# Optimization experiments

Measured on AMD Instinct MI355X. Metric: run time of the kernel, lower is better.

## Reference

```python
import jax, jax.numpy as jnp
import numpy as np

T = 64        # time steps (batch)
N_SIDE = 256  # grid side, N = N_SIDE**2 flattened grid points
HID = 32      # hidden width of the shared per-point MLP
IN_CH = 5     # 5-point periodic stencil (l, l2, center, r, r2)


def _stencil_gather(x, n):
    """Replicates MLPConv._preprocess / make_px / get_value exactly.

    x: [T, n*n] flattened periodic grid. Returns [T, n*n, 5].
    get_value wraps indices via the piecewise rule (v-n if v>=n) and relies on
    numpy negative flat indexing for v=-1, which is the final `% (n*n)` here.
    Output position i_loop*n + j_loop reads grid flat index (j_loop+ik) + n*(i_loop+jk).
    """
    ii = jnp.arange(n)[:, None]  # i_loop (outer loop in make_px)
    jj = jnp.arange(n)[None, :]  # j_loop (inner loop)

    def idx(ik, jk):
        a = jj + ik
        a = jnp.where(a >= n, a - n, a)
        b = ii + jk
        b = jnp.where(b >= n, b - n, b)
        return ((a + n * b) % (n * n)).reshape(-1)  # [n*n]

    # channel order from _preprocess: cat([l, l2, px, r, r2], -1)
    offsets = [(-1, 0), (0, -1), (0, 0), (1, 0), (0, 1)]
    cols = jnp.stack([idx(ik, jk) for ik, jk in offsets], axis=-1)  # [n*n, 5]
    return x[:, cols]  # [T, n*n, 5]


def setup_inputs() -> dict:
    key = jax.random.key(0)
    ks = jax.random.split(key, 7)
    n2 = N_SIDE * N_SIDE
    x = jax.random.normal(ks[0], (T, n2), dtype=jnp.float32)
    # torch Linear weights are [out, in]; we store transposed [in, out] for x @ W.
    # Original init: xavier_normal * 10, bias zeros; scaled normals are equivalent for a baseline.
    def w(k, fan_in, fan_out):
        std = 10.0 * np.sqrt(2.0 / (fan_in + fan_out))
        return std * jax.random.normal(k, (fan_in, fan_out), dtype=jnp.float32)
    return {
        "x": x,
        "W0": w(ks[1], IN_CH, HID), "b0": jnp.zeros((HID,), jnp.float32),
        "W1": w(ks[2], HID, HID),   "b1": jnp.zeros((HID,), jnp.float32),
        "W2": w(ks[3], HID, 1),     "b2": jnp.zeros((1,), jnp.float32),
    }


def reference(x, W0, b0, W1, b1, W2, b2):
    # Note: the x_copy dual path in the torch forward never affects the returned
    # tensor (dead code), so the faithful math is a plain 3-layer MLP over the
    # 5-point periodic stencil gather, ELU between layers, no final activation.
    n = int(np.sqrt(x.shape[1]))
    px = _stencil_gather(x, n)                 # [T, N, 5]
    h = jax.nn.elu(px @ W0 + b0)               # [T, N, HID]
    h = jax.nn.elu(h @ W1 + b1)                # [T, N, HID]
    out = h @ W2 + b2                          # [T, N, 1]
    return out.squeeze(-1)                     # [T, N] (matches res.squeeze())
```

## Files before the change

### kernel.cpp

```cpp
#include <hip/hip_runtime.h>
#include <hip/hip_bf16.h>

#define T_STEPS 64
#define NS 256
#define N2 (NS * NS)
#define HID 32

typedef _Float16 half8 __attribute__((ext_vector_type(8)));
typedef float float4v __attribute__((ext_vector_type(4)));

#define TILES_TOTAL (T_STEPS * (N2 / 16))
#define TPW 16
#define WAVES_PER_BLOCK 4
#define NBLOCKS (TILES_TOTAL / (TPW * WAVES_PER_BLOCK))

__device__ __forceinline__ float elu(float z) {
    return (z > 0.0f) ? z : (__expf(z) - 1.0f);
}

__global__ __launch_bounds__(256) void mlpconv_mfma_kernel(
    const float* __restrict__ x,
    const float* __restrict__ W0, const float* __restrict__ b0,
    const float* __restrict__ W1, const float* __restrict__ b1,
    const float* __restrict__ W2, const float* __restrict__ b2,
    float* __restrict__ out)
{
    const int lane = threadIdx.x & 63;
    const int wid  = threadIdx.x >> 6;
    const int m    = lane & 15;
    const int kg   = lane >> 4;

    float w0c[5][8];
    #pragma unroll
    for (int c = 0; c < 5; ++c)
        #pragma unroll
        for (int i = 0; i < 8; ++i)
            w0c[c][i] = W0[c * HID + kg * 8 + i];
    float b0v[8];
    #pragma unroll
    for (int i = 0; i < 8; ++i) b0v[i] = b0[kg * 8 + i];

    half8 a0, a1;
    #pragma unroll
    for (int i = 0; i < 8; ++i) {
        a0[i] = (_Float16)W1[(kg * 8 + i) * HID + m];
        a1[i] = (_Float16)W1[(kg * 8 + i) * HID + 16 + m];
    }
    float4v c0i, c1i;
    #pragma unroll
    for (int r = 0; r < 4; ++r) {
        c0i[r] = b1[kg * 4 + r];
        c1i[r] = b1[16 + kg * 4 + r];
    }
    float w2a[4], w2b[4];
    #pragma unroll
    for (int r = 0; r < 4; ++r) {
        w2a[r] = W2[kg * 4 + r];
        w2b[r] = W2[16 + kg * 4 + r];
    }
    const float b2v = b2[0];

    const int gw = blockIdx.x * WAVES_PER_BLOCK + wid;
    const int g0 = gw * TPW;

    for (int l = 0; l < TPW; ++l) {
        const int g  = g0 + l;
        const int t  = g >> 12;
        const int s0 = (g & 4095) << 4;
        const int s  = s0 + m;
        const float* xt = x + ((size_t)t << 16);

        const int sl  = (s - 1)  & (N2 - 1);
        const int sl2 = (s - NS) & (N2 - 1);
        const int sr  = (s & ~(NS - 1)) | ((s + 1) & (NS - 1));
        const int sr2 = (s + NS) & (N2 - 1);

        const float in0 = xt[sl];
        const float in1 = xt[sl2];
        const float in2 = xt[s];
        const float in3 = xt[sr];
        const float in4 = xt[sr2];

        half8 hfrag;
        #pragma unroll
        for (int i = 0; i < 8; ++i) {
            float z = b0v[i];
            z = fmaf(in0, w0c[0][i], z);
            z = fmaf(in1, w0c[1][i], z);
            z = fmaf(in2, w0c[2][i], z);
            z = fmaf(in3, w0c[3][i], z);
            z = fmaf(in4, w0c[4][i], z);
            hfrag[i] = (_Float16)elu(z);
        }

        float4v d0 = __builtin_amdgcn_mfma_f32_16x16x32_f16(a0, hfrag, c0i, 0, 0, 0);
        float4v d1 = __builtin_amdgcn_mfma_f32_16x16x32_f16(a1, hfrag, c1i, 0, 0, 0);

        float part = 0.0f;
        #pragma unroll
        for (int r = 0; r < 4; ++r) {
            part = fmaf(elu(d0[r]), w2a[r], part);
            part = fmaf(elu(d1[r]), w2b[r], part);
        }
        part += __shfl_xor(part, 16, 64);
        part += __shfl_xor(part, 32, 64);

        if (kg == 0) {
            out[((size_t)t << 16) + s] = part + b2v;
        }
    }
}

extern "C" void kernel_launch(void* const* d_in, const int* in_sizes, int n_in,
                              void* d_out, int out_size, void* d_ws, size_t ws_size,
                              hipStream_t stream) {
    const float* x  = (const float*)d_in[0];
    const float* W0 = (const float*)d_in[1];
    const float* b0 = (const float*)d_in[2];
    const float* W1 = (const float*)d_in[3];
    const float* b1 = (const float*)d_in[4];
    const float* W2 = (const float*)d_in[5];
    const float* b2 = (const float*)d_in[6];
    float* out = (float*)d_out;

    mlpconv_mfma_kernel<<<dim3(NBLOCKS), dim3(256), 0, stream>>>(
        x, W0, b0, W1, b1, W2, b2, out);
}
```

Before: 149.8 us.

## Use packed fp16 first layer, branchless ELU, and row-per-wave stencil addressing

Moves the first-layer computation and its ELU to packed half2 arithmetic, which halves VALU instruction count. The outer ELU becomes branchless using min/max. Each wave now processes one grid row, with a 2D grid indexed by row block and time step. Interior rows use fixed-offset loads in a fully unrolled loop with no per-element wrap masking, while the two boundary rows keep the general path. This trades fp16 precision in layer 0 for fewer ALU ops and simpler address math.

```diff
diff --git a/kernel.cpp b/kernel.cpp
--- a/kernel.cpp
+++ b/kernel.cpp
@@ -1,24 +1,34 @@
 #include <hip/hip_runtime.h>
-#include <hip/hip_bf16.h>
+#include <hip/hip_fp16.h>
 
-#define T_STEPS 64
 #define NS 256
 #define N2 (NS * NS)
 #define HID 32
+#define T_STEPS 64
 
-typedef _Float16 half8 __attribute__((ext_vector_type(8)));
-typedef float float4v __attribute__((ext_vector_type(4)));
+typedef _Float16 h2     __attribute__((ext_vector_type(2)));
+typedef _Float16 half8  __attribute__((ext_vector_type(8)));
+typedef float    float4v __attribute__((ext_vector_type(4)));
 
-#define TILES_TOTAL (T_STEPS * (N2 / 16))
-#define TPW 16
-#define WAVES_PER_BLOCK 4
-#define NBLOCKS (TILES_TOTAL / (TPW * WAVES_PER_BLOCK))
-
-__device__ __forceinline__ float elu(float z) {
-    return (z > 0.0f) ? z : (__expf(z) - 1.0f);
+__device__ __forceinline__ float eluf(float z) {
+    return fmaxf(z, __expf(fminf(z, 0.0f)) - 1.0f);
 }
 
-__global__ __launch_bounds__(256) void mlpconv_mfma_kernel(
+__device__ __forceinline__ h2 splat2(float f) {
+    _Float16 h = (_Float16)f;
+    h2 r; r[0] = h; r[1] = h;
+    return r;
+}
+
+__device__ __forceinline__ h2 elu2(h2 z) {
+    h2 zero; zero[0] = (_Float16)0.f; zero[1] = (_Float16)0.f;
+    h2 zm = __builtin_elementwise_min(z, zero);
+    h2 e  = __builtin_elementwise_exp2(zm * (_Float16)1.442695041f);
+    h2 em1 = e + (_Float16)(-1.0f);
+    return __builtin_elementwise_max(z, em1);
+}
+
+__global__ __launch_bounds__(256, 4) void mlpconv_row_kernel(
     const float* __restrict__ x,
     const float* __restrict__ W0, const float* __restrict__ b0,
     const float* __restrict__ W1, const float* __restrict__ b1,
@@ -26,19 +36,34 @@
     float* __restrict__ out)
 {
     const int lane = threadIdx.x & 63;
-    const int wid  = threadIdx.x >> 6;
     const int m    = lane & 15;
     const int kg   = lane >> 4;
 
-    float w0c[5][8];
-    #pragma unroll
-    for (int c = 0; c < 5; ++c)
-        #pragma unroll
-        for (int i = 0; i < 8; ++i)
-            w0c[c][i] = W0[c * HID + kg * 8 + i];
-    float b0v[8];
-    #pragma unroll
-    for (int i = 0; i < 8; ++i) b0v[i] = b0[kg * 8 + i];
+    h2 w00, w01, w02, w03, w10, w11, w12, w13, w20, w21, w22, w23,
+       w30, w31, w32, w33, w40, w41, w42, w43;
+    {
+        const int c0 = kg * 8;
+        #define LW(c, v0, v1, v2, v3)                                   \
+            v0[0] = (_Float16)W0[c * HID + c0 + 0];                     \
+            v0[1] = (_Float16)W0[c * HID + c0 + 1];                     \
+            v1[0] = (_Float16)W0[c * HID + c0 + 2];                     \
+            v1[1] = (_Float16)W0[c * HID + c0 + 3];                     \
+            v2[0] = (_Float16)W0[c * HID + c0 + 4];                     \
+            v2[1] = (_Float16)W0[c * HID + c0 + 5];                     \
+            v3[0] = (_Float16)W0[c * HID + c0 + 6];                     \
+            v3[1] = (_Float16)W0[c * HID + c0 + 7];
+        LW(0, w00, w01, w02, w03)
+        LW(1, w10, w11, w12, w13)
+        LW(2, w20, w21, w22, w23)
+        LW(3, w30, w31, w32, w33)
+        LW(4, w40, w41, w42, w43)
+        #undef LW
+    }
+    h2 b00, b01, b02, b03;
+    b00[0] = (_Float16)b0[kg * 8 + 0]; b00[1] = (_Float16)b0[kg * 8 + 1];
+    b01[0] = (_Float16)b0[kg * 8 + 2]; b01[1] = (_Float16)b0[kg * 8 + 3];
+    b02[0] = (_Float16)b0[kg * 8 + 4]; b02[1] = (_Float16)b0[kg * 8 + 5];
+    b03[0] = (_Float16)b0[kg * 8 + 6]; b03[1] = (_Float16)b0[kg * 8 + 7];
 
     half8 a0, a1;
     #pragma unroll
@@ -47,68 +72,87 @@
         a1[i] = (_Float16)W1[(kg * 8 + i) * HID + 16 + m];
     }
     float4v c0i, c1i;
+    float w2a0, w2a1, w2a2, w2a3, w2b0, w2b1, w2b2, w2b3;
     #pragma unroll
     for (int r = 0; r < 4; ++r) {
         c0i[r] = b1[kg * 4 + r];
         c1i[r] = b1[16 + kg * 4 + r];
     }
-    float w2a[4], w2b[4];
-    #pragma unroll
-    for (int r = 0; r < 4; ++r) {
-        w2a[r] = W2[kg * 4 + r];
-        w2b[r] = W2[16 + kg * 4 + r];
-    }
+    w2a0 = W2[kg * 4 + 0]; w2a1 = W2[kg * 4 + 1];
+    w2a2 = W2[kg * 4 + 2]; w2a3 = W2[kg * 4 + 3];
+    w2b0 = W2[16 + kg * 4 + 0]; w2b1 = W2[16 + kg * 4 + 1];
+    w2b2 = W2[16 + kg * 4 + 2]; w2b3 = W2[16 + kg * 4 + 3];
     const float b2v = b2[0];
 
-    const int gw = blockIdx.x * WAVES_PER_BLOCK + wid;
-    const int g0 = gw * TPW;
+    const int wid = __builtin_amdgcn_readfirstlane(threadIdx.x >> 6);
+    const int t   = blockIdx.y;
+    const int i0  = blockIdx.x * 4 + wid;
+    const int sbase = i0 << 8;
 
-    for (int l = 0; l < TPW; ++l) {
-        const int g  = g0 + l;
-        const int t  = g >> 12;
-        const int s0 = (g & 4095) << 4;
-        const int s  = s0 + m;
-        const float* xt = x + ((size_t)t << 16);
+    const float* __restrict__ xt   = x   + ((size_t)t << 16);
+    float* __restrict__       outt = out + ((size_t)t << 16);
 
-        const int sl  = (s - 1)  & (N2 - 1);
-        const int sl2 = (s - NS) & (N2 - 1);
-        const int sr  = (s & ~(NS - 1)) | ((s + 1) & (NS - 1));
-        const int sr2 = (s + NS) & (N2 - 1);
+    #define TILE_BODY(IN0, IN1, IN2, IN3, IN4, OUTP)                      \
+    {                                                                     \
+        h2 z0 = b00, z1v = b01, z2 = b02, z3 = b03;                       \
+        h2 p;                                                             \
+        p = splat2(IN0); z0 = p * w00 + z0; z1v = p * w01 + z1v;          \
+                         z2 = p * w02 + z2; z3 = p * w03 + z3;            \
+        p = splat2(IN1); z0 = p * w10 + z0; z1v = p * w11 + z1v;          \
+                         z2 = p * w12 + z2; z3 = p * w13 + z3;            \
+        p = splat2(IN2); z0 = p * w20 + z0; z1v = p * w21 + z1v;          \
+                         z2 = p * w22 + z2; z3 = p * w23 + z3;            \
+        p = splat2(IN3); z0 = p * w30 + z0; z1v = p * w31 + z1v;          \
+                         z2 = p * w32 + z2; z3 = p * w33 + z3;            \
+        p = splat2(IN4); z0 = p * w40 + z0; z1v = p * w41 + z1v;          \
+                         z2 = p * w42 + z2; z3 = p * w43 + z3;            \
+        h2 h0p = elu2(z0), h1p = elu2(z1v), h2p = elu2(z2), h3p = elu2(z3);\
+        half8 hf;                                                         \
+        hf[0] = h0p[0]; hf[1] = h0p[1]; hf[2] = h1p[0]; hf[3] = h1p[1];   \
+        hf[4] = h2p[0]; hf[5] = h2p[1]; hf[6] = h3p[0]; hf[7] = h3p[1];   \
+        float4v d0 = __builtin_amdgcn_mfma_f32_16x16x32_f16(a0, hf, c0i, 0, 0, 0); \
+        float4v d1 = __builtin_amdgcn_mfma_f32_16x16x32_f16(a1, hf, c1i, 0, 0, 0); \
+        float part = 0.0f;                                                \
+        part = fmaf(eluf(d0[0]), w2a0, part);                             \
+        part = fmaf(eluf(d0[1]), w2a1, part);                             \
+        part = fmaf(eluf(d0[2]), w2a2, part);                             \
+        part = fmaf(eluf(d0[3]), w2a3, part);                             \
+        part = fmaf(eluf(d1[0]), w2b0, part);                             \
+        part = fmaf(eluf(d1[1]), w2b1, part);                             \
+        part = fmaf(eluf(d1[2]), w2b2, part);                             \
+        part = fmaf(eluf(d1[3]), w2b3, part);                             \
+        part += __shfl_xor(part, 16, 64);                                 \
+        part += __shfl_xor(part, 32, 64);                                 \
+        if (kg == 0) *(OUTP) = part + b2v;                                \
+    }
 
-        const float in0 = xt[sl];
-        const float in1 = xt[sl2];
-        const float in2 = xt[s];
-        const float in3 = xt[sr];
-        const float in4 = xt[sr2];
-
-        half8 hfrag;
+    if (i0 != 0 && i0 != 255) {
+        const float* __restrict__ bp = xt + sbase + m;
+        const float rowwrap = xt[sbase];
         #pragma unroll
-        for (int i = 0; i < 8; ++i) {
-            float z = b0v[i];
-            z = fmaf(in0, w0c[0][i], z);
-            z = fmaf(in1, w0c[1][i], z);
-            z = fmaf(in2, w0c[2][i], z);
-            z = fmaf(in3, w0c[3][i], z);
-            z = fmaf(in4, w0c[4][i], z);
-            hfrag[i] = (_Float16)elu(z);
+        for (int l = 0; l < 15; ++l) {
+            const int o = 16 * l;
+            TILE_BODY(bp[o - 1], bp[o - NS], bp[o], bp[o + 1], bp[o + NS],
+                      outt + sbase + o + m)
         }
-
-        float4v d0 = __builtin_amdgcn_mfma_f32_16x16x32_f16(a0, hfrag, c0i, 0, 0, 0);
-        float4v d1 = __builtin_amdgcn_mfma_f32_16x16x32_f16(a1, hfrag, c1i, 0, 0, 0);
-
-        float part = 0.0f;
+        {
+            const int o = 16 * 15;
+            const float in3 = (m == 15) ? rowwrap : bp[o + 1];
+            TILE_BODY(bp[o - 1], bp[o - NS], bp[o], in3, bp[o + NS],
+                      outt + sbase + o + m)
+        }
+    } else {
         #pragma unroll
-        for (int r = 0; r < 4; ++r) {
-            part = fmaf(elu(d0[r]), w2a[r], part);
-            part = fmaf(elu(d1[r]), w2b[r], part);
-        }
-        part += __shfl_xor(part, 16, 64);
-        part += __shfl_xor(part, 32, 64);
-
-        if (kg == 0) {
-            out[((size_t)t << 16) + s] = part + b2v;
+        for (int l = 0; l < 16; ++l) {
+            const int s   = sbase + 16 * l + m;
+            const int sl  = (s - 1)  & (N2 - 1);
+            const int sl2 = (s - NS) & (N2 - 1);
+            const int sr  = (s & ~(NS - 1)) | ((s + 1) & (NS - 1));
+            const int sr2 = (s + NS) & (N2 - 1);
+            TILE_BODY(xt[sl], xt[sl2], xt[s], xt[sr], xt[sr2], outt + s)
         }
     }
+    #undef TILE_BODY
 }
 
 extern "C" void kernel_launch(void* const* d_in, const int* in_sizes, int n_in,
@@ -123,6 +167,7 @@
     const float* b2 = (const float*)d_in[6];
     float* out = (float*)d_out;
 
-    mlpconv_mfma_kernel<<<dim3(NBLOCKS), dim3(256), 0, stream>>>(
+    dim3 grid(NS / 4, T_STEPS);
+    mlpconv_row_kernel<<<grid, dim3(256), 0, stream>>>(
         x, W0, b0, W1, b1, W2, b2, out);
 }
```

Result: faster. 140.2 us (-6.4%).
